# Performance work log

Measured on AMD Instinct MI355X. Metric: run time of the kernel, lower is better.

Reference implementation:

```python
import jax, jax.numpy as jnp
import numpy as np

N_NODES = 50000
N_EDGES = 800000
D_FEAT = 128
HIDDEN = 256
N_CLASSES = 2


def setup_inputs() -> dict:
    key = jax.random.key(0)
    ks = jax.random.split(key, 9)
    x = jax.random.normal(ks[0], (N_NODES, D_FEAT), dtype=jnp.float32)
    edge_index = jax.random.randint(ks[1], (2, N_EDGES), 0, N_NODES, dtype=jnp.int32)
    # SAGEConv params: lin_l (applied to aggregated neighbors), lin_r (root), bias
    s1 = 1.0 / np.sqrt(D_FEAT)
    s2 = 1.0 / np.sqrt(HIDDEN)
    W1l = jax.random.normal(ks[2], (D_FEAT, HIDDEN), dtype=jnp.float32) * s1
    W1r = jax.random.normal(ks[3], (D_FEAT, HIDDEN), dtype=jnp.float32) * s1
    b1 = jax.random.normal(ks[4], (HIDDEN,), dtype=jnp.float32) * s1
    W2l = jax.random.normal(ks[5], (HIDDEN, N_CLASSES), dtype=jnp.float32) * s2
    W2r = jax.random.normal(ks[6], (HIDDEN, N_CLASSES), dtype=jnp.float32) * s2
    b2 = jax.random.normal(ks[7], (N_CLASSES,), dtype=jnp.float32) * s2
    return {"x": x, "edge_index": edge_index, "W1l": W1l, "W1r": W1r,
            "b1": b1, "W2l": W2l, "W2r": W2r, "b2": b2}


def _sage_conv(x, src, dst, Wl, Wr, b):
    # mean-aggregate neighbor features x[src] into destination nodes
    n = x.shape[0]
    agg = jax.ops.segment_sum(x[src], dst, num_segments=n)  # [N, d]
    deg = jax.ops.segment_sum(jnp.ones((src.shape[0],), x.dtype), dst,
                              num_segments=n)
    mean = agg / jnp.maximum(deg, 1.0)[:, None]
    return mean @ Wl + x @ Wr + b


def reference(x, edge_index, W1l, W1r, b1, W2l, W2r, b2):
    src, dst = edge_index[0], edge_index[1]
    h = jax.nn.relu(_sage_conv(x, src, dst, W1l, W1r, b1))
    embeddings = h  # dropout is identity in eval mode
    out = jax.nn.sigmoid(_sage_conv(embeddings, src, dst, W2l, W2r, b2))
    return out, embeddings
```

## Files before the change

kernel.cpp:

```cpp
#include <hip/hip_runtime.h>
#include <math.h>

#define N_NODES 50000
#define N_EDGES 800000
#define D_FEAT 128
#define HIDDEN 256
#define NB_SCAN 196
#define GEMM_BLOCKS 782

#define PREP_CVT_B 512
#define PREP_CNT_B 256
#define PREP_WF_B 64
#define FILL_B 512
#define AGG_B 2048

typedef __bf16 bf16x8 __attribute__((ext_vector_type(8)));
typedef float f32x4 __attribute__((ext_vector_type(4)));

__device__ __forceinline__ unsigned f2b(float f) {
    unsigned u = __builtin_bit_cast(unsigned, f);
    return (u + 0x7fff + ((u >> 16) & 1)) >> 16;
}

__global__ __launch_bounds__(256) void prep(
    const float* __restrict__ x, const int* __restrict__ dst,
    const float* __restrict__ W1l, const float* __restrict__ W1r,
    unsigned* __restrict__ Arow, int* __restrict__ cnt,
    unsigned short* __restrict__ Wfrag) {
    int b = blockIdx.x;
    int t = threadIdx.x;
    if (b < PREP_CVT_B) {
        for (int g = b * 256 + t; g < 800000; g += PREP_CVT_B * 256) {
            float4 v0 = *(const float4*)(x + (size_t)g * 8);
            float4 v1 = *(const float4*)(x + (size_t)g * 8 + 4);
            uint4 o;
            o.x = f2b(v0.x) | (f2b(v0.y) << 16);
            o.y = f2b(v0.z) | (f2b(v0.w) << 16);
            o.z = f2b(v1.x) | (f2b(v1.y) << 16);
            o.w = f2b(v1.z) | (f2b(v1.w) << 16);
            int d = g >> 4;
            int j = (g << 2) & 63;
            *(uint4*)(Arow + (size_t)d * 128 + 64 + j) = o;
        }
    } else if (b < PREP_CVT_B + PREP_CNT_B) {
        for (int e = (b - PREP_CVT_B) * 256 + t; e < N_EDGES; e += PREP_CNT_B * 256)
            atomicAdd(&cnt[dst[e]], 1);
    } else {
        for (int tt = (b - PREP_CVT_B - PREP_CNT_B) * 256 + t; tt < 65536;
             tt += PREP_WF_B * 256) {
            int j = tt & 7;
            int lane = (tt >> 3) & 63;
            int ks = (tt >> 9) & 7;
            int nt = tt >> 12;
            int k = ks * 32 + ((lane >> 4) << 3) + j;
            int n = (nt << 4) + (lane & 15);
            float v = (k < 128) ? W1l[k * 256 + n] : W1r[(k - 128) * 256 + n];
            Wfrag[tt] = (unsigned short)f2b(v);
        }
    }
}

__global__ void scan1(const int* __restrict__ cnt, int* __restrict__ bsum) {
    __shared__ int tmp[256];
    int t = threadIdx.x;
    int i = blockIdx.x * 256 + t;
    tmp[t] = (i < N_NODES) ? cnt[i] : 0;
    __syncthreads();
    for (int off = 128; off > 0; off >>= 1) {
        if (t < off) tmp[t] += tmp[t + off];
        __syncthreads();
    }
    if (t == 0) bsum[blockIdx.x] = tmp[0];
}

__global__ void scanB(const int* __restrict__ cnt, const int* __restrict__ bsum,
                      int* __restrict__ rowpos) {
    __shared__ int bs[256];
    __shared__ int tmp[256];
    int t = threadIdx.x;
    int b = blockIdx.x;
    bs[t] = (t < NB_SCAN) ? bsum[t] : 0;
    __syncthreads();
    for (int off = 1; off < 256; off <<= 1) {
        int y = (t >= off) ? bs[t - off] : 0;
        __syncthreads();
        bs[t] += y;
        __syncthreads();
    }
    int boff = (b == 0) ? 0 : bs[b - 1];
    int i = b * 256 + t;
    int v = (i < N_NODES) ? cnt[i] : 0;
    tmp[t] = v;
    __syncthreads();
    for (int off = 1; off < 256; off <<= 1) {
        int y = (t >= off) ? tmp[t - off] : 0;
        __syncthreads();
        tmp[t] += y;
        __syncthreads();
    }
    if (i < N_NODES) rowpos[i] = tmp[t] - v + boff;
}

__global__ __launch_bounds__(256) void fill_kernel(
    const int* __restrict__ src, const int* __restrict__ dst,
    int* __restrict__ rowpos, unsigned short* __restrict__ esrc) {
    for (int e = blockIdx.x * 256 + threadIdx.x; e < N_EDGES; e += FILL_B * 256) {
        int pos = atomicAdd(&rowpos[dst[e]], 1);
        esrc[pos] = (unsigned short)src[e];
    }
}

__global__ __launch_bounds__(256) void agg1(
    const unsigned* __restrict__ Arow_x, unsigned* __restrict__ Arow_m,
    const unsigned short* __restrict__ esrc,
    const int* __restrict__ rowend, const int* __restrict__ cnt) {
    int wid = (blockIdx.x * 256 + threadIdx.x) >> 6;
    int lane = threadIdx.x & 63;
    for (int d = wid; d < N_NODES; d += AGG_B * 4) {
        int end = rowend[d];
        int c = cnt[d];
        float a0 = 0.0f, a1 = 0.0f;
        for (int base = end - c; base < end; base += 64) {
            int m = end - base; if (m > 64) m = 64;
            int idx = base + lane;
            int e = (int)esrc[idx < end ? idx : end - 1];
            for (int j0 = 0; j0 < m; j0 += 8) {
#pragma unroll
                for (int j = 0; j < 8; j++) {
                    int s = __shfl(e, j0 + j);
                    unsigned u = Arow_x[(size_t)s * 128 + 64 + lane];
                    float sc = (j0 + j < m) ? 1.0f : 0.0f;
                    a0 += sc * __builtin_bit_cast(float, u << 16);
                    a1 += sc * __builtin_bit_cast(float, u & 0xffff0000u);
                }
            }
        }
        float inv = 1.0f / fmaxf((float)c, 1.0f);
        Arow_m[(size_t)d * 128 + lane] = f2b(a0 * inv) | (f2b(a1 * inv) << 16);
    }
}

__global__ __launch_bounds__(256) void gemm1ps(
    const unsigned* __restrict__ Arow, const unsigned short* __restrict__ Wfrag,
    const float* __restrict__ b1, const float* __restrict__ W2l,
    const float* __restrict__ W2r, const float* __restrict__ b2,
    float* __restrict__ h, float* __restrict__ p, float* __restrict__ s) {
    __shared__ unsigned A[64 * 128];
    __shared__ float ppart[64][4];

    int r0 = blockIdx.x * 64;
    int tid = threadIdx.x;
    int w = tid >> 6;
    int lane = tid & 63;
    int quad = lane >> 4;
    int l15 = lane & 15;

    ((float*)ppart)[tid] = 0.0f;

    int sr = tid >> 2;
    int cb = (tid & 3) << 3;
#pragma unroll
    for (int j = 0; j < 8; j++) {
        int c = cb + j;
        uint4 v = *(const uint4*)(Arow + (size_t)(r0 + sr) * 128 + (c << 2));
        int cp = c ^ (sr & 7);
        *(uint4*)(A + sr * 128 + (cp << 2)) = v;
    }
    __syncthreads();

    f32x4 acc[16];
#pragma unroll
    for (int i = 0; i < 16; i++) acc[i] = (f32x4){0.0f, 0.0f, 0.0f, 0.0f};

    for (int ks = 0; ks < 8; ks++) {
        bf16x8 bfr[4];
#pragma unroll
        for (int nt = 0; nt < 4; nt++) {
            int ntg = (w << 2) + nt;
            uint4 raw = *(const uint4*)(Wfrag + ((((ntg << 3) + ks) << 6) + lane) * 8);
            bfr[nt] = __builtin_bit_cast(bf16x8, raw);
        }
#pragma unroll
        for (int mt = 0; mt < 4; mt++) {
            int row = (mt << 4) + l15;
            int c = (ks << 2) + quad;
            uint4 araw = *(const uint4*)(A + row * 128 + ((c ^ (row & 7)) << 2));
            bf16x8 afr = __builtin_bit_cast(bf16x8, araw);
#pragma unroll
            for (int nt = 0; nt < 4; nt++) {
                acc[(mt << 2) + nt] = __builtin_amdgcn_mfma_f32_16x16x32_bf16(
                    afr, bfr[nt], acc[(mt << 2) + nt], 0, 0, 0);
            }
        }
    }

    float w2[4][4];
#pragma unroll
    for (int nt = 0; nt < 4; nt++) {
        int col = (w << 6) + (nt << 4) + l15;
        float2 l2 = *(const float2*)(W2l + col * 2);
        float2 r2 = *(const float2*)(W2r + col * 2);
        w2[nt][0] = l2.x; w2[nt][1] = l2.y; w2[nt][2] = r2.x; w2[nt][3] = r2.y;
    }

#pragma unroll
    for (int mt = 0; mt < 4; mt++) {
        float red[4][4];
#pragma unroll
        for (int v = 0; v < 4; v++)
#pragma unroll
            for (int r = 0; r < 4; r++) red[v][r] = 0.0f;

#pragma unroll
        for (int nt = 0; nt < 4; nt++) {
            int col = (w << 6) + (nt << 4) + l15;
            float b = b1[col];
            f32x4 v = acc[(mt << 2) + nt];
#pragma unroll
            for (int r = 0; r < 4; r++) {
                float hv = v[r] + b;
                hv = hv > 0.0f ? hv : 0.0f;
                int row = r0 + (mt << 4) + (quad << 2) + r;
                if (row < N_NODES) h[(size_t)row * 256 + col] = hv;
                red[0][r] += hv * w2[nt][0];
                red[1][r] += hv * w2[nt][1];
                red[2][r] += hv * w2[nt][2];
                red[3][r] += hv * w2[nt][3];
            }
        }
#pragma unroll
        for (int v = 0; v < 4; v++)
#pragma unroll
            for (int r = 0; r < 4; r++) {
                red[v][r] += __shfl_xor(red[v][r], 1);
                red[v][r] += __shfl_xor(red[v][r], 2);
                red[v][r] += __shfl_xor(red[v][r], 4);
                red[v][r] += __shfl_xor(red[v][r], 8);
            }
        if (l15 == 0) {
            int lrow = (mt << 4) + (quad << 2);
#pragma unroll
            for (int r = 0; r < 4; r++)
#pragma unroll
                for (int v = 0; v < 4; v++)
                    atomicAdd(&ppart[lrow + r][v], red[v][r]);
        }
    }
    __syncthreads();

    if (tid < 64) {
        int row = r0 + tid;
        if (row < N_NODES) {
            float2 pv = {ppart[tid][0], ppart[tid][1]};
            float2 sv = {ppart[tid][2] + b2[0], ppart[tid][3] + b2[1]};
            *(float2*)(p + (size_t)row * 2) = pv;
            *(float2*)(s + (size_t)row * 2) = sv;
        }
    }
}

__global__ __launch_bounds__(256) void agg2(
    const float* __restrict__ p, const float* __restrict__ s,
    const unsigned short* __restrict__ esrc,
    const int* __restrict__ rowend, const int* __restrict__ cnt,
    float* __restrict__ out) {
    int wid = (blockIdx.x * 256 + threadIdx.x) >> 6;
    int lane = threadIdx.x & 63;
    for (int d = wid; d < N_NODES; d += AGG_B * 4) {
        int end = rowend[d];
        int c = cnt[d];
        float a0 = 0.0f, a1 = 0.0f;
        for (int base = end - c; base < end; base += 64) {
            int idx = base + lane;
            if (idx < end) {
                int ss = (int)esrc[idx];
                float2 v = *(const float2*)(p + (size_t)ss * 2);
                a0 += v.x; a1 += v.y;
            }
        }
#pragma unroll
        for (int off = 32; off > 0; off >>= 1) {
            a0 += __shfl_down(a0, off);
            a1 += __shfl_down(a1, off);
        }
        if (lane == 0) {
            float inv = 1.0f / fmaxf((float)c, 1.0f);
            float z0 = a0 * inv + s[(size_t)d * 2 + 0];
            float z1 = a1 * inv + s[(size_t)d * 2 + 1];
            float2 o = {1.0f / (1.0f + expf(-z0)), 1.0f / (1.0f + expf(-z1))};
            *(float2*)(out + (size_t)d * 2) = o;
        }
    }
}

extern "C" void kernel_launch(void* const* d_in, const int* in_sizes, int n_in,
                              void* d_out, int out_size, void* d_ws, size_t ws_size,
                              hipStream_t stream) {
    const float* x   = (const float*)d_in[0];
    const int*   ei  = (const int*)d_in[1];
    const float* W1l = (const float*)d_in[2];
    const float* W1r = (const float*)d_in[3];
    const float* b1  = (const float*)d_in[4];
    const float* W2l = (const float*)d_in[5];
    const float* W2r = (const float*)d_in[6];
    const float* b2  = (const float*)d_in[7];

    const int* src = ei;
    const int* dst = ei + N_EDGES;

    float* out = (float*)d_out;
    float* emb = out + (size_t)N_NODES * 2;

    int* cnt    = (int*)d_ws;
    int* rowpos = cnt + N_NODES;
    int* bsum   = rowpos + N_NODES;
    unsigned short* esrc = (unsigned short*)(bsum + 256);
    unsigned* Arow = (unsigned*)(esrc + 800064);
    unsigned short* Wfrag = (unsigned short*)(Arow + (size_t)50048 * 128);
    float* p = (float*)(Wfrag + 65536);
    float* s = p + (size_t)N_NODES * 2;

    hipMemsetAsync(cnt, 0, N_NODES * sizeof(int), stream);

    prep<<<PREP_CVT_B + PREP_CNT_B + PREP_WF_B, 256, 0, stream>>>(
        x, dst, W1l, W1r, Arow, cnt, Wfrag);

    scan1<<<NB_SCAN, 256, 0, stream>>>(cnt, bsum);
    scanB<<<NB_SCAN, 256, 0, stream>>>(cnt, bsum, rowpos);
    fill_kernel<<<FILL_B, 256, 0, stream>>>(src, dst, rowpos, esrc);

    agg1<<<AGG_B, 256, 0, stream>>>(Arow, Arow, esrc, rowpos, cnt);

    gemm1ps<<<GEMM_BLOCKS, 256, 0, stream>>>(Arow, Wfrag, b1, W2l, W2r, b2, emb, p, s);

    agg2<<<AGG_B, 256, 0, stream>>>(p, s, esrc, rowpos, cnt, out);
}
```

Measured before the change: 260.0 us.

## Fuse neighbor mean aggregation into first-layer GEMM blocks

Removes the separate agg1 kernel. Each 512-thread GEMM block now gathers and averages neighbor rows for its 64 nodes directly into the swizzled LDS A tile, alongside the node's own bf16 features. The bf16 x buffer becomes a compact 64-word-per-row array, and the 256 output columns are split across 8 waves with a one-step register prefetch of the weight fragments. This avoids writing and re-reading the mean matrix and one kernel launch. The cost is that irregular gather latency now sits inside the GEMM block ahead of its MFMA work.

```diff
diff --git a/kernel.cpp b/kernel.cpp
--- a/kernel.cpp
+++ b/kernel.cpp
@@ -25,7 +25,7 @@
 __global__ __launch_bounds__(256) void prep(
     const float* __restrict__ x, const int* __restrict__ dst,
     const float* __restrict__ W1l, const float* __restrict__ W1r,
-    unsigned* __restrict__ Arow, int* __restrict__ cnt,
+    unsigned* __restrict__ xb, int* __restrict__ cnt,
     unsigned short* __restrict__ Wfrag) {
     int b = blockIdx.x;
     int t = threadIdx.x;
@@ -39,8 +39,8 @@
             o.z = f2b(v1.x) | (f2b(v1.y) << 16);
             o.w = f2b(v1.z) | (f2b(v1.w) << 16);
             int d = g >> 4;
-            int j = (g << 2) & 63;
-            *(uint4*)(Arow + (size_t)d * 128 + 64 + j) = o;
+            int j = (g & 15) << 2;
+            *(uint4*)(xb + (size_t)d * 64 + j) = o;
         }
     } else if (b < PREP_CVT_B + PREP_CNT_B) {
         for (int e = (b - PREP_CVT_B) * 256 + t; e < N_EDGES; e += PREP_CNT_B * 256)
@@ -110,40 +110,12 @@
     }
 }
 
-__global__ __launch_bounds__(256) void agg1(
-    const unsigned* __restrict__ Arow_x, unsigned* __restrict__ Arow_m,
-    const unsigned short* __restrict__ esrc,
-    const int* __restrict__ rowend, const int* __restrict__ cnt) {
-    int wid = (blockIdx.x * 256 + threadIdx.x) >> 6;
-    int lane = threadIdx.x & 63;
-    for (int d = wid; d < N_NODES; d += AGG_B * 4) {
-        int end = rowend[d];
-        int c = cnt[d];
-        float a0 = 0.0f, a1 = 0.0f;
-        for (int base = end - c; base < end; base += 64) {
-            int m = end - base; if (m > 64) m = 64;
-            int idx = base + lane;
-            int e = (int)esrc[idx < end ? idx : end - 1];
-            for (int j0 = 0; j0 < m; j0 += 8) {
-#pragma unroll
-                for (int j = 0; j < 8; j++) {
-                    int s = __shfl(e, j0 + j);
-                    unsigned u = Arow_x[(size_t)s * 128 + 64 + lane];
-                    float sc = (j0 + j < m) ? 1.0f : 0.0f;
-                    a0 += sc * __builtin_bit_cast(float, u << 16);
-                    a1 += sc * __builtin_bit_cast(float, u & 0xffff0000u);
-                }
-            }
-        }
-        float inv = 1.0f / fmaxf((float)c, 1.0f);
-        Arow_m[(size_t)d * 128 + lane] = f2b(a0 * inv) | (f2b(a1 * inv) << 16);
-    }
-}
-
-__global__ __launch_bounds__(256) void gemm1ps(
-    const unsigned* __restrict__ Arow, const unsigned short* __restrict__ Wfrag,
-    const float* __restrict__ b1, const float* __restrict__ W2l,
-    const float* __restrict__ W2r, const float* __restrict__ b2,
+__global__ __launch_bounds__(512) void gemm1ps(
+    const unsigned* __restrict__ xb, const unsigned short* __restrict__ esrc,
+    const int* __restrict__ rowend, const int* __restrict__ cnt,
+    const unsigned short* __restrict__ Wfrag, const float* __restrict__ b1,
+    const float* __restrict__ W2l, const float* __restrict__ W2r,
+    const float* __restrict__ b2,
     float* __restrict__ h, float* __restrict__ p, float* __restrict__ s) {
     __shared__ unsigned A[64 * 128];
     __shared__ float ppart[64][4];
@@ -155,30 +127,61 @@
     int quad = lane >> 4;
     int l15 = lane & 15;
 
-    ((float*)ppart)[tid] = 0.0f;
-
-    int sr = tid >> 2;
-    int cb = (tid & 3) << 3;
-#pragma unroll
-    for (int j = 0; j < 8; j++) {
-        int c = cb + j;
-        uint4 v = *(const uint4*)(Arow + (size_t)(r0 + sr) * 128 + (c << 2));
-        int cp = c ^ (sr & 7);
-        *(uint4*)(A + sr * 128 + (cp << 2)) = v;
-    }
-    __syncthreads();
-
-    f32x4 acc[16];
-#pragma unroll
-    for (int i = 0; i < 16; i++) acc[i] = (f32x4){0.0f, 0.0f, 0.0f, 0.0f};
+    if (tid < 256) ((float*)ppart)[tid] = 0.0f;
+
+    int cm = lane >> 2;
+    int cx = 16 + (lane >> 2);
+    int wo = lane & 3;
+    for (int rr = 0; rr < 8; rr++) {
+        int lr = (w << 3) + rr;
+        int d = r0 + lr;
+        unsigned mword = 0, xword = 0;
+        if (d < N_NODES) {
+            int end = rowend[d];
+            int c = cnt[d];
+            float a0 = 0.0f, a1 = 0.0f;
+            for (int base = end - c; base < end; base += 64) {
+                int m = end - base; if (m > 64) m = 64;
+                int idx = base + lane;
+                int e = (int)esrc[idx < end ? idx : end - 1];
+                for (int j0 = 0; j0 < m; j0 += 8) {
+#pragma unroll
+                    for (int j = 0; j < 8; j++) {
+                        int ss = __shfl(e, j0 + j);
+                        unsigned u = xb[(size_t)ss * 64 + lane];
+                        float sc = (j0 + j < m) ? 1.0f : 0.0f;
+                        a0 += sc * __builtin_bit_cast(float, u << 16);
+                        a1 += sc * __builtin_bit_cast(float, u & 0xffff0000u);
+                    }
+                }
+            }
+            float inv = 1.0f / fmaxf((float)c, 1.0f);
+            mword = f2b(a0 * inv) | (f2b(a1 * inv) << 16);
+            xword = xb[(size_t)d * 64 + lane];
+        }
+        A[lr * 128 + ((cm ^ (lr & 7)) << 2) + wo] = mword;
+        A[lr * 128 + ((cx ^ (lr & 7)) << 2) + wo] = xword;
+    }
+    __syncthreads();
+
+    f32x4 acc[8];
+#pragma unroll
+    for (int i = 0; i < 8; i++) acc[i] = (f32x4){0.0f, 0.0f, 0.0f, 0.0f};
+
+    uint4 braw[2];
+#pragma unroll
+    for (int nt = 0; nt < 2; nt++)
+        braw[nt] = *(const uint4*)(Wfrag + ((((w * 2 + nt) << 3) + 0) * 64 + lane) * 8);
 
     for (int ks = 0; ks < 8; ks++) {
-        bf16x8 bfr[4];
-#pragma unroll
-        for (int nt = 0; nt < 4; nt++) {
-            int ntg = (w << 2) + nt;
-            uint4 raw = *(const uint4*)(Wfrag + ((((ntg << 3) + ks) << 6) + lane) * 8);
-            bfr[nt] = __builtin_bit_cast(bf16x8, raw);
+        bf16x8 bfr[2];
+        bfr[0] = __builtin_bit_cast(bf16x8, braw[0]);
+        bfr[1] = __builtin_bit_cast(bf16x8, braw[1]);
+        if (ks < 7) {
+#pragma unroll
+            for (int nt = 0; nt < 2; nt++)
+                braw[nt] = *(const uint4*)(
+                    Wfrag + ((((w * 2 + nt) << 3) + ks + 1) * 64 + lane) * 8);
         }
 #pragma unroll
         for (int mt = 0; mt < 4; mt++) {
@@ -187,17 +190,17 @@
             uint4 araw = *(const uint4*)(A + row * 128 + ((c ^ (row & 7)) << 2));
             bf16x8 afr = __builtin_bit_cast(bf16x8, araw);
 #pragma unroll
-            for (int nt = 0; nt < 4; nt++) {
-                acc[(mt << 2) + nt] = __builtin_amdgcn_mfma_f32_16x16x32_bf16(
-                    afr, bfr[nt], acc[(mt << 2) + nt], 0, 0, 0);
-            }
-        }
-    }
-
-    float w2[4][4];
-#pragma unroll
-    for (int nt = 0; nt < 4; nt++) {
-        int col = (w << 6) + (nt << 4) + l15;
+            for (int nt = 0; nt < 2; nt++) {
+                acc[(mt << 1) + nt] = __builtin_amdgcn_mfma_f32_16x16x32_bf16(
+                    afr, bfr[nt], acc[(mt << 1) + nt], 0, 0, 0);
+            }
+        }
+    }
+
+    float w2[2][4];
+#pragma unroll
+    for (int nt = 0; nt < 2; nt++) {
+        int col = (w << 5) + (nt << 4) + l15;
         float2 l2 = *(const float2*)(W2l + col * 2);
         float2 r2 = *(const float2*)(W2r + col * 2);
         w2[nt][0] = l2.x; w2[nt][1] = l2.y; w2[nt][2] = r2.x; w2[nt][3] = r2.y;
@@ -212,10 +215,10 @@
             for (int r = 0; r < 4; r++) red[v][r] = 0.0f;
 
 #pragma unroll
-        for (int nt = 0; nt < 4; nt++) {
-            int col = (w << 6) + (nt << 4) + l15;
+        for (int nt = 0; nt < 2; nt++) {
+            int col = (w << 5) + (nt << 4) + l15;
             float b = b1[col];
-            f32x4 v = acc[(mt << 2) + nt];
+            f32x4 v = acc[(mt << 1) + nt];
 #pragma unroll
             for (int r = 0; r < 4; r++) {
                 float hv = v[r] + b;
@@ -315,23 +318,22 @@
     int* rowpos = cnt + N_NODES;
     int* bsum   = rowpos + N_NODES;
     unsigned short* esrc = (unsigned short*)(bsum + 256);
-    unsigned* Arow = (unsigned*)(esrc + 800064);
-    unsigned short* Wfrag = (unsigned short*)(Arow + (size_t)50048 * 128);
+    unsigned* xb = (unsigned*)(esrc + 800064);
+    unsigned short* Wfrag = (unsigned short*)(xb + (size_t)N_NODES * 64);
     float* p = (float*)(Wfrag + 65536);
     float* s = p + (size_t)N_NODES * 2;
 
     hipMemsetAsync(cnt, 0, N_NODES * sizeof(int), stream);
 
     prep<<<PREP_CVT_B + PREP_CNT_B + PREP_WF_B, 256, 0, stream>>>(
-        x, dst, W1l, W1r, Arow, cnt, Wfrag);
+        x, dst, W1l, W1r, xb, cnt, Wfrag);
 
     scan1<<<NB_SCAN, 256, 0, stream>>>(cnt, bsum);
     scanB<<<NB_SCAN, 256, 0, stream>>>(cnt, bsum, rowpos);
     fill_kernel<<<FILL_B, 256, 0, stream>>>(src, dst, rowpos, esrc);
 
-    agg1<<<AGG_B, 256, 0, stream>>>(Arow, Arow, esrc, rowpos, cnt);
-
-    gemm1ps<<<GEMM_BLOCKS, 256, 0, stream>>>(Arow, Wfrag, b1, W2l, W2r, b2, emb, p, s);
+    gemm1ps<<<GEMM_BLOCKS, 512, 0, stream>>>(xb, esrc, rowpos, cnt, Wfrag,
+                                             b1, W2l, W2r, b2, emb, p, s);
 
     agg2<<<AGG_B, 256, 0, stream>>>(p, s, esrc, rowpos, cnt, out);
 }
```

Measured after the change: 281.9 us. 1.08x slower.

## Split bf16 x and mean into compact arrays and halve GEMM row tile

Applied to the files above, without the earlier changes.

The interleaved 128-word Arow buffer is replaced by two separate 64-word-per-row bf16 arrays: xb for x and mb for the aggregated mean. In agg1 each neighbour gather now reads a dense 256-byte row instead of half of a 512-byte stride, which should make cache-line use tighter. gemm1ps now tiles 32 rows per block instead of 64, which doubles the block count and halves the accumulator registers, so occupancy should rise at the cost of loading the weight fragments twice as often. The h output is written with nontemporal stores so it does not pollute the cache.

```diff
diff --git a/kernel.cpp b/kernel.cpp
--- a/kernel.cpp
+++ b/kernel.cpp
@@ -6,7 +6,7 @@
 #define D_FEAT 128
 #define HIDDEN 256
 #define NB_SCAN 196
-#define GEMM_BLOCKS 782
+#define GEMM_BLOCKS 1563
 
 #define PREP_CVT_B 512
 #define PREP_CNT_B 256
@@ -25,7 +25,7 @@
 __global__ __launch_bounds__(256) void prep(
     const float* __restrict__ x, const int* __restrict__ dst,
     const float* __restrict__ W1l, const float* __restrict__ W1r,
-    unsigned* __restrict__ Arow, int* __restrict__ cnt,
+    unsigned* __restrict__ xb, int* __restrict__ cnt,
     unsigned short* __restrict__ Wfrag) {
     int b = blockIdx.x;
     int t = threadIdx.x;
@@ -39,8 +39,8 @@
             o.z = f2b(v1.x) | (f2b(v1.y) << 16);
             o.w = f2b(v1.z) | (f2b(v1.w) << 16);
             int d = g >> 4;
-            int j = (g << 2) & 63;
-            *(uint4*)(Arow + (size_t)d * 128 + 64 + j) = o;
+            int j = (g & 15) << 2;
+            *(uint4*)(xb + (size_t)d * 64 + j) = o;
         }
     } else if (b < PREP_CVT_B + PREP_CNT_B) {
         for (int e = (b - PREP_CVT_B) * 256 + t; e < N_EDGES; e += PREP_CNT_B * 256)
@@ -111,7 +111,7 @@
 }
 
 __global__ __launch_bounds__(256) void agg1(
-    const unsigned* __restrict__ Arow_x, unsigned* __restrict__ Arow_m,
+    const unsigned* __restrict__ xb, unsigned* __restrict__ mb,
     const unsigned short* __restrict__ esrc,
     const int* __restrict__ rowend, const int* __restrict__ cnt) {
     int wid = (blockIdx.x * 256 + threadIdx.x) >> 6;
@@ -127,8 +127,8 @@
             for (int j0 = 0; j0 < m; j0 += 8) {
 #pragma unroll
                 for (int j = 0; j < 8; j++) {
-                    int s = __shfl(e, j0 + j);
-                    unsigned u = Arow_x[(size_t)s * 128 + 64 + lane];
+                    int ss = __shfl(e, j0 + j);
+                    unsigned u = xb[(size_t)ss * 64 + lane];
                     float sc = (j0 + j < m) ? 1.0f : 0.0f;
                     a0 += sc * __builtin_bit_cast(float, u << 16);
                     a1 += sc * __builtin_bit_cast(float, u & 0xffff0000u);
@@ -136,41 +136,44 @@
             }
         }
         float inv = 1.0f / fmaxf((float)c, 1.0f);
-        Arow_m[(size_t)d * 128 + lane] = f2b(a0 * inv) | (f2b(a1 * inv) << 16);
+        mb[(size_t)d * 64 + lane] = f2b(a0 * inv) | (f2b(a1 * inv) << 16);
     }
 }
 
 __global__ __launch_bounds__(256) void gemm1ps(
-    const unsigned* __restrict__ Arow, const unsigned short* __restrict__ Wfrag,
-    const float* __restrict__ b1, const float* __restrict__ W2l,
-    const float* __restrict__ W2r, const float* __restrict__ b2,
+    const unsigned* __restrict__ mb, const unsigned* __restrict__ xb,
+    const unsigned short* __restrict__ Wfrag, const float* __restrict__ b1,
+    const float* __restrict__ W2l, const float* __restrict__ W2r,
+    const float* __restrict__ b2,
     float* __restrict__ h, float* __restrict__ p, float* __restrict__ s) {
-    __shared__ unsigned A[64 * 128];
-    __shared__ float ppart[64][4];
-
-    int r0 = blockIdx.x * 64;
+    __shared__ unsigned A[32 * 128];
+    __shared__ float ppart[32][4];
+
+    int r0 = blockIdx.x * 32;
     int tid = threadIdx.x;
     int w = tid >> 6;
     int lane = tid & 63;
     int quad = lane >> 4;
     int l15 = lane & 15;
 
-    ((float*)ppart)[tid] = 0.0f;
-
-    int sr = tid >> 2;
-    int cb = (tid & 3) << 3;
-#pragma unroll
-    for (int j = 0; j < 8; j++) {
-        int c = cb + j;
-        uint4 v = *(const uint4*)(Arow + (size_t)(r0 + sr) * 128 + (c << 2));
+    if (tid < 128) ((float*)ppart)[tid] = 0.0f;
+
+    int sr = tid >> 3;
+    int c0 = tid & 7;
+#pragma unroll
+    for (int j = 0; j < 4; j++) {
+        int c = c0 + (j << 3);
+        uint4 v;
+        if (c < 16) v = *(const uint4*)(mb + (size_t)(r0 + sr) * 64 + (c << 2));
+        else        v = *(const uint4*)(xb + (size_t)(r0 + sr) * 64 + ((c - 16) << 2));
         int cp = c ^ (sr & 7);
         *(uint4*)(A + sr * 128 + (cp << 2)) = v;
     }
     __syncthreads();
 
-    f32x4 acc[16];
-#pragma unroll
-    for (int i = 0; i < 16; i++) acc[i] = (f32x4){0.0f, 0.0f, 0.0f, 0.0f};
+    f32x4 acc[8];
+#pragma unroll
+    for (int i = 0; i < 8; i++) acc[i] = (f32x4){0.0f, 0.0f, 0.0f, 0.0f};
 
     for (int ks = 0; ks < 8; ks++) {
         bf16x8 bfr[4];
@@ -181,7 +184,7 @@
             bfr[nt] = __builtin_bit_cast(bf16x8, raw);
         }
 #pragma unroll
-        for (int mt = 0; mt < 4; mt++) {
+        for (int mt = 0; mt < 2; mt++) {
             int row = (mt << 4) + l15;
             int c = (ks << 2) + quad;
             uint4 araw = *(const uint4*)(A + row * 128 + ((c ^ (row & 7)) << 2));
@@ -204,7 +207,7 @@
     }
 
 #pragma unroll
-    for (int mt = 0; mt < 4; mt++) {
+    for (int mt = 0; mt < 2; mt++) {
         float red[4][4];
 #pragma unroll
         for (int v = 0; v < 4; v++)
@@ -221,7 +224,8 @@
                 float hv = v[r] + b;
                 hv = hv > 0.0f ? hv : 0.0f;
                 int row = r0 + (mt << 4) + (quad << 2) + r;
-                if (row < N_NODES) h[(size_t)row * 256 + col] = hv;
+                if (row < N_NODES)
+                    __builtin_nontemporal_store(hv, &h[(size_t)row * 256 + col]);
                 red[0][r] += hv * w2[nt][0];
                 red[1][r] += hv * w2[nt][1];
                 red[2][r] += hv * w2[nt][2];
@@ -248,7 +252,7 @@
     }
     __syncthreads();
 
-    if (tid < 64) {
+    if (tid < 32) {
         int row = r0 + tid;
         if (row < N_NODES) {
             float2 pv = {ppart[tid][0], ppart[tid][1]};
@@ -315,23 +319,25 @@
     int* rowpos = cnt + N_NODES;
     int* bsum   = rowpos + N_NODES;
     unsigned short* esrc = (unsigned short*)(bsum + 256);
-    unsigned* Arow = (unsigned*)(esrc + 800064);
-    unsigned short* Wfrag = (unsigned short*)(Arow + (size_t)50048 * 128);
+    unsigned* xb = (unsigned*)(esrc + 800064);
+    unsigned* mb = xb + (size_t)50048 * 64;
+    unsigned short* Wfrag = (unsigned short*)(mb + (size_t)50048 * 64);
     float* p = (float*)(Wfrag + 65536);
     float* s = p + (size_t)N_NODES * 2;
 
     hipMemsetAsync(cnt, 0, N_NODES * sizeof(int), stream);
 
     prep<<<PREP_CVT_B + PREP_CNT_B + PREP_WF_B, 256, 0, stream>>>(
-        x, dst, W1l, W1r, Arow, cnt, Wfrag);
+        x, dst, W1l, W1r, xb, cnt, Wfrag);
 
     scan1<<<NB_SCAN, 256, 0, stream>>>(cnt, bsum);
     scanB<<<NB_SCAN, 256, 0, stream>>>(cnt, bsum, rowpos);
     fill_kernel<<<FILL_B, 256, 0, stream>>>(src, dst, rowpos, esrc);
 
-    agg1<<<AGG_B, 256, 0, stream>>>(Arow, Arow, esrc, rowpos, cnt);
-
-    gemm1ps<<<GEMM_BLOCKS, 256, 0, stream>>>(Arow, Wfrag, b1, W2l, W2r, b2, emb, p, s);
+    agg1<<<AGG_B, 256, 0, stream>>>(xb, mb, esrc, rowpos, cnt);
+
+    gemm1ps<<<GEMM_BLOCKS, 256, 0, stream>>>(mb, xb, Wfrag, b1, W2l, W2r, b2,
+                                             emb, p, s);
 
     agg2<<<AGG_B, 256, 0, stream>>>(p, s, esrc, rowpos, cnt, out);
 }
```

Result: no change. 259.0 us (-0.4%).
